# Optimization experiments

Hardware: AMD Instinct MI355X
Metric: run time of the kernel (lower is better)

The kernel has to match this reference:

```python
import jax, jax.numpy as jnp
from jax import lax
import numpy as np

B, T, D, H, FC, OUT = 256, 512, 64, 512, 512, 8


def _uniform(key, shape, scale):
    return jax.random.uniform(key, shape, jnp.float32, -scale, scale)


def setup_inputs() -> dict:
    key = jax.random.key(0)
    ks = jax.random.split(key, 16)
    s = 1.0 / np.sqrt(H)
    inp = {
        "x": jax.random.normal(ks[0], (B, T, D), jnp.float32),
        # LSTM layer 0 (PyTorch gate order i,f,g,o stacked along 4H)
        "W_ih0": _uniform(ks[1], (4 * H, D), s),
        "W_hh0": _uniform(ks[2], (4 * H, H), s),
        "b_ih0": _uniform(ks[3], (4 * H,), s),
        "b_hh0": _uniform(ks[4], (4 * H,), s),
        # LSTM layer 1
        "W_ih1": _uniform(ks[5], (4 * H, H), s),
        "W_hh1": _uniform(ks[6], (4 * H, H), s),
        "b_ih1": _uniform(ks[7], (4 * H,), s),
        "b_hh1": _uniform(ks[8], (4 * H,), s),
        # MLP head: Linear(H,FC) -> ReLU -> Linear(FC,OUT)
        "W_fc1": _uniform(ks[9], (FC, H), s),
        "b_fc1": _uniform(ks[10], (FC,), s),
        "W_fc2": _uniform(ks[11], (OUT, FC), 1.0 / np.sqrt(FC)),
        "b_fc2": _uniform(ks[12], (OUT,), 1.0 / np.sqrt(FC)),
    }
    return inp


def _lstm_layer(x, W_ih, W_hh, b_ih, b_hh):
    # x: [B, T, Din] -> hidden sequence [B, T, H]
    Bn, Tn, _ = x.shape
    Hn = W_hh.shape[1]
    # precompute input-to-gate projections for all timesteps (one big GEMM)
    xg = jnp.einsum('btd,gd->btg', x, W_ih) + b_ih + b_hh  # [B, T, 4H]

    def step(carry, xg_t):
        h, c = carry
        g = xg_t + h @ W_hh.T  # [B, 4H]
        i, f, gg, o = jnp.split(g, 4, axis=-1)
        c = jax.nn.sigmoid(f) * c + jax.nn.sigmoid(i) * jnp.tanh(gg)
        h = jax.nn.sigmoid(o) * jnp.tanh(c)
        return (h, c), h

    h0 = jnp.zeros((Bn, Hn), x.dtype)
    (_, _), hs = lax.scan(step, (h0, h0), jnp.swapaxes(xg, 0, 1))  # hs: [T, B, H]
    return jnp.swapaxes(hs, 0, 1)


def reference(x, W_ih0, W_hh0, b_ih0, b_hh0, W_ih1, W_hh1, b_ih1, b_hh1,
              W_fc1, b_fc1, W_fc2, b_fc2):
    h = _lstm_layer(x, W_ih0, W_hh0, b_ih0, b_hh0)
    h = _lstm_layer(h, W_ih1, W_hh1, b_ih1, b_hh1)
    last = h[:, -1, :]  # [B, H]
    z = jax.nn.relu(last @ W_fc1.T + b_fc1)
    return z @ W_fc2.T + b_fc2  # [B, OUT]
```

## Files before the change

kernel.cpp:

```cpp
#include <hip/hip_runtime.h>
#include <math.h>

typedef unsigned short u16;
typedef __attribute__((ext_vector_type(8))) short short8;
typedef __attribute__((ext_vector_type(4))) float float4v;

#define HH   512
#define BB   256
#define TLEN 512
#define DD   64

__device__ __forceinline__ float sigm(float x) { return 1.0f / (1.0f + __expf(-x)); }

__device__ __forceinline__ u16 bf16rn(float v) {
    unsigned u = __float_as_uint(v);
    u += 0x7fffu + ((u >> 16) & 1u);
    return (u16)(u >> 16);
}
__device__ __forceinline__ float bf16tf(u16 h) { return __uint_as_float(((unsigned)h) << 16); }


__global__ __launch_bounds__(256) void split_kernel(const float* __restrict__ src,
                                                    u16* __restrict__ hi, u16* __restrict__ lo, int n)
{
    for (int i = blockIdx.x * 256 + threadIdx.x; i < n; i += gridDim.x * 256) {
        float v = src[i];
        u16 h = bf16rn(v);
        hi[i] = h;
        lo[i] = bf16rn(v - bf16tf(h));
    }
}

__global__ __launch_bounds__(256) void zero_kernel(unsigned* p, int n)
{
    int i = blockIdx.x * 256 + threadIdx.x;
    if (i < n) p[i] = 0u;
}


template<int NKT, int C1, bool ROLE1>
__device__ void lstm_body(
    const u16* __restrict__ X1h, const u16* __restrict__ X1l,
    const u16* __restrict__ B1h, const u16* __restrict__ B1l, const int ldb1,
    const u16* __restrict__ B2h, const u16* __restrict__ B2l,
    const float* __restrict__ pbi, const float* __restrict__ pbh,
    u16* __restrict__ h0hA, u16* __restrict__ h0lA,
    u16* __restrict__ h0hB, u16* __restrict__ h0lB,
    u16* __restrict__ h1hA, u16* __restrict__ h1lA,
    u16* __restrict__ h1hB, u16* __restrict__ h1lB,
    float* __restrict__ h1last,
    unsigned* bcnt, unsigned* bgen,
    const int m0, const int j0, u16* smem)
{
    const int tid  = threadIdx.x;
    const int lane = tid & 63;
    const int wv   = tid >> 6;
    const int g    = wv & 3;
    const int kh   = wv >> 2;
    float* sX = (float*)smem;

    short8 rBh[NKT], rBl[NKT];
    {
        const size_t brow = (size_t)(g * HH + j0 + (lane & 15));
        const int kq = (lane >> 4) * 8;
#pragma unroll
        for (int i = 0; i < NKT; ++i) {
            const int kt = kh * NKT + i;
            const u16 *ph, *pl;
            if (kt < C1) {
                ph = B1h + brow * (size_t)ldb1 + kt * 32 + kq;
                pl = B1l + brow * (size_t)ldb1 + kt * 32 + kq;
            } else {
                ph = B2h + brow * HH + (size_t)(kt - C1) * 32 + kq;
                pl = B2l + brow * HH + (size_t)(kt - C1) * 32 + kq;
            }
            rBh[i] = *(const short8*)ph;
            rBl[i] = *(const short8*)pl;
        }
    }

    int r_[2], ks_[2], hl_[2], half_[2], loff_[2];
#pragma unroll
    for (int q = 0; q < 2; ++q) {
        const int idx  = q * 512 + tid;
        const int tile = idx >> 8;
        half_[q] = tile >> 1;
        hl_[q]   = tile & 1;
        const int t8 = idx & 255;
        const int r  = t8 >> 2;
        const int k3 = t8 & 3;
        r_[q]  = r;
        ks_[q] = k3 * 8;
        loff_[q] = tile * 2048 + r * 32 + ((k3 ^ ((r >> 1) & 3)) * 8);
    }

    const int cR = lane & 15, q4 = lane >> 4;
    const int abase = kh * 4096 + cR * 32 + ((q4 ^ ((cR >> 1) & 3)) * 8);

    const int jj  = j0 + (tid & 15);
    const int mb2 = (tid >> 4) * 2;
    const float bI = pbi[jj] + pbh[jj];
    const float bF = pbi[HH + jj] + pbh[HH + jj];
    const float bG = pbi[2 * HH + jj] + pbh[2 * HH + jj];
    const float bO = pbi[3 * HH + jj] + pbh[3 * HH + jj];
    float cst0 = 0.f, cst1 = 0.f;

    for (int n = 0; n <= TLEN; ++n) {
        const int rb = n & 1;
        const bool active = ROLE1 ? (n > 0) : (n < TLEN);
        if (active) {
            const u16 *A1h_, *A1l_, *A2h_, *A2l_;
            u16 *wh, *wl;
            size_t ld1;
            if (ROLE1) {
                A1h_ = rb ? h0hB : h0hA; A1l_ = rb ? h0lB : h0lA;
                A2h_ = rb ? h1hB : h1hA; A2l_ = rb ? h1lB : h1lA;
                wh   = rb ? h1hA : h1hB; wl   = rb ? h1lA : h1lB;
                ld1 = HH;
            } else {
                A1h_ = X1h + (size_t)n * DD; A1l_ = X1l + (size_t)n * DD;
                A2h_ = rb ? h0hB : h0hA;     A2l_ = rb ? h0lB : h0lA;
                wh   = rb ? h0hA : h0hB;     wl   = rb ? h0lA : h0lB;
                ld1 = (size_t)TLEN * DD;
            }

            auto srcp = [&](int kt, int r, int ks, int lo) -> const u16* {
                if (kt < C1) return (lo ? A1l_ : A1h_) + (size_t)(m0 + r) * ld1 + kt * 32 + ks;
                return (lo ? A2l_ : A2h_) + (size_t)(m0 + r) * HH + (size_t)(kt - C1) * 32 + ks;
            };

            float4v acc[4];
#pragma unroll
            for (int mt = 0; mt < 4; ++mt) acc[mt] = (float4v){0.f, 0.f, 0.f, 0.f};

            short8 vS[2][2];
            vS[0][0] = *(const short8*)srcp(half_[0] * NKT + 0, r_[0], ks_[0], hl_[0]);
            vS[0][1] = *(const short8*)srcp(half_[1] * NKT + 0, r_[1], ks_[1], hl_[1]);
            if (NKT > 1) {
                vS[1][0] = *(const short8*)srcp(half_[0] * NKT + 1, r_[0], ks_[0], hl_[0]);
                vS[1][1] = *(const short8*)srcp(half_[1] * NKT + 1, r_[1], ks_[1], hl_[1]);
            }
            *(short8*)&smem[loff_[0]] = vS[0][0];
            *(short8*)&smem[loff_[1]] = vS[0][1];

#pragma unroll
            for (int i = 0; i < NKT; ++i) {
                __syncthreads();
                const int buf = i & 1;
                if (i + 1 < NKT) {
                    *(short8*)&smem[(buf ^ 1) * 8192 + loff_[0]] = vS[(i + 1) & 1][0];
                    *(short8*)&smem[(buf ^ 1) * 8192 + loff_[1]] = vS[(i + 1) & 1][1];
                }
                if (i + 2 < NKT) {
                    vS[i & 1][0] = *(const short8*)srcp(half_[0] * NKT + i + 2, r_[0], ks_[0], hl_[0]);
                    vS[i & 1][1] = *(const short8*)srcp(half_[1] * NKT + i + 2, r_[1], ks_[1], hl_[1]);
                }
                const int ab = buf * 8192 + abase;
                short8 aH[4], aL[4];
#pragma unroll
                for (int mt = 0; mt < 4; ++mt) {
                    aH[mt] = *(const short8*)&smem[ab + mt * 512];
                    aL[mt] = *(const short8*)&smem[ab + 2048 + mt * 512];
                }
#pragma unroll
                for (int mt = 0; mt < 4; ++mt) {
                    acc[mt] = __builtin_amdgcn_mfma_f32_16x16x32_bf16(aH[mt], rBh[i], acc[mt], 0, 0, 0);
                    acc[mt] = __builtin_amdgcn_mfma_f32_16x16x32_bf16(aH[mt], rBl[i], acc[mt], 0, 0, 0);
                    acc[mt] = __builtin_amdgcn_mfma_f32_16x16x32_bf16(aL[mt], rBh[i], acc[mt], 0, 0, 0);
                }
            }

            __syncthreads();
#pragma unroll
            for (int mt = 0; mt < 4; ++mt)
#pragma unroll
                for (int r = 0; r < 4; ++r)
                    sX[wv * 1152 + (mt * 16 + (lane >> 4) * 4 + r) * 18 + (lane & 15)] = acc[mt][r];
            __syncthreads();

#pragma unroll
            for (int p = 0; p < 2; ++p) {
                const int m = mb2 + p;
                const int xb = m * 18 + (tid & 15);
                const float gi = sX[0 * 1152 + xb] + sX[4 * 1152 + xb] + bI;
                const float gf = sX[1 * 1152 + xb] + sX[5 * 1152 + xb] + bF;
                const float gg = sX[2 * 1152 + xb] + sX[6 * 1152 + xb] + bG;
                const float go = sX[3 * 1152 + xb] + sX[7 * 1152 + xb] + bO;
                const float cp = p ? cst1 : cst0;
                const float cn = sigm(gf) * cp + sigm(gi) * tanhf(gg);
                const float h  = sigm(go) * tanhf(cn);
                if (p) cst1 = cn; else cst0 = cn;
                const size_t off = (size_t)(m0 + m) * HH + jj;
                const u16 hv = bf16rn(h);
                wh[off] = hv;
                wl[off] = bf16rn(h - bf16tf(hv));
                if (ROLE1 && n == TLEN) h1last[off] = h;
            }
        }

        __syncthreads();
        if (tid == 0) {
            const unsigned g0 = __hip_atomic_load(bgen, __ATOMIC_RELAXED, __HIP_MEMORY_SCOPE_AGENT);
            const unsigned a = __hip_atomic_fetch_add(bcnt, 1u, __ATOMIC_RELEASE, __HIP_MEMORY_SCOPE_AGENT);
            if (a == 63u) {
                __hip_atomic_store(bcnt, 0u, __ATOMIC_RELAXED, __HIP_MEMORY_SCOPE_AGENT);
                __hip_atomic_store(bgen, g0 + 1u, __ATOMIC_RELEASE, __HIP_MEMORY_SCOPE_AGENT);
            } else {
                int sp = 0;
                while (__hip_atomic_load(bgen, __ATOMIC_RELAXED, __HIP_MEMORY_SCOPE_AGENT) == g0) {
                    __builtin_amdgcn_s_sleep(2);
                    if ((++sp & 63) == 0)
                        (void)__hip_atomic_load(bgen, __ATOMIC_ACQUIRE, __HIP_MEMORY_SCOPE_AGENT);
                }
            }
            (void)__hip_atomic_load(bgen, __ATOMIC_ACQUIRE, __HIP_MEMORY_SCOPE_AGENT);
        }
        __syncthreads();
    }
}

__global__ __launch_bounds__(512, 2) void lstm_persistent(
    const u16* __restrict__ xhi, const u16* __restrict__ xlo,
    const u16* __restrict__ Wih0h, const u16* __restrict__ Wih0l,
    const u16* __restrict__ Whh0h, const u16* __restrict__ Whh0l,
    const u16* __restrict__ Wih1h, const u16* __restrict__ Wih1l,
    const u16* __restrict__ Whh1h, const u16* __restrict__ Whh1l,
    const float* __restrict__ bi0, const float* __restrict__ bh0,
    const float* __restrict__ bi1, const float* __restrict__ bh1,
    u16* h0hA, u16* h0lA, u16* h0hB, u16* h0lB,
    u16* h1hA, u16* h1lA, u16* h1hB, u16* h1lB,
    float* __restrict__ h1last, unsigned* bar)
{
    __shared__ u16 smem[18432];
    const bool role1 = (blockIdx.x >= 128);
    const int idx = blockIdx.x & 127;
    const int m0 = (idx & 3) * 64;
    const int j0 = (idx >> 2) * 16;
    const int gid = idx & 3;
    unsigned* bcnt = bar + gid * 64;
    unsigned* bgen = bar + gid * 64 + 32;

    if (role1)
        lstm_body<16, 16, true>(nullptr, nullptr,
            Wih1h, Wih1l, HH, Whh1h, Whh1l, bi1, bh1,
            h0hA, h0lA, h0hB, h0lB, h1hA, h1lA, h1hB, h1lB,
            h1last, bcnt, bgen, m0, j0, smem);
    else
        lstm_body<9, 2, false>(xhi, xlo,
            Wih0h, Wih0l, DD, Whh0h, Whh0l, bi0, bh0,
            h0hA, h0lA, h0hB, h0lB, h1hA, h1lA, h1hB, h1lB,
            nullptr, bcnt, bgen, m0, j0, smem);
}


template <int MODE>
__global__ __launch_bounds__(256) void gemm_step(
    const float* __restrict__ A1, int lda1, int K1, const float* __restrict__ W1,
    const float* __restrict__ A2, int K2, const float* __restrict__ W2,
    const float* __restrict__ b1, const float* __restrict__ b2,
    const float* __restrict__ c_in, float* __restrict__ c_out,
    float* __restrict__ h_out)
{
    __shared__ float sA[16][33];
    __shared__ float sW[128][33];

    const int tid = threadIdx.x;
    const int tj  = tid & 31;
    const int tg  = tid >> 5;
    const int m0  = blockIdx.x * 16;
    const int j0  = blockIdx.y * ((MODE == 0) ? 32 : 128);

    float acc[2][4] = {{0.f, 0.f, 0.f, 0.f}, {0.f, 0.f, 0.f, 0.f}};

    for (int seg = 0; seg < 2; ++seg) {
        const float* A  = seg ? A2 : A1;
        const float* W  = seg ? W2 : W1;
        const int    K  = seg ? K2 : K1;
        const int    ld = seg ? HH : lda1;
        if (K == 0) continue;
        for (int kb = 0; kb < K; kb += 32) {
            __syncthreads();
            {
                int idxq = tid;
#pragma unroll
                for (int r = 0; r < 2; ++r, idxq += 256) {
                    int row = idxq >> 5, col = idxq & 31;
                    sA[row][col] = A[(m0 + row) * ld + kb + col];
                }
            }
            {
#pragma unroll
                for (int i = 0; i < 16; ++i) {
                    int idxq = i * 256 + tid;
                    int row = idxq >> 5, col = idxq & 31;
                    int grw;
                    if (MODE == 0) grw = (row >> 5) * HH + j0 + (row & 31);
                    else           grw = j0 + row;
                    sW[row][col] = W[grw * K + kb + col];
                }
            }
            __syncthreads();
#pragma unroll
            for (int k = 0; k < 32; ++k) {
                float a0 = sA[tg][k];
                float a1 = sA[tg + 8][k];
                float w0 = sW[tj][k];
                float w1 = sW[32 + tj][k];
                float w2 = sW[64 + tj][k];
                float w3 = sW[96 + tj][k];
                acc[0][0] += a0 * w0; acc[0][1] += a0 * w1;
                acc[0][2] += a0 * w2; acc[0][3] += a0 * w3;
                acc[1][0] += a1 * w0; acc[1][1] += a1 * w1;
                acc[1][2] += a1 * w2; acc[1][3] += a1 * w3;
            }
        }
    }

    if (MODE == 0) {
        const int j = j0 + tj;
        const float bi = b1[j] + b2[j];
        const float bf = b1[HH + j] + b2[HH + j];
        const float bg = b1[2 * HH + j] + b2[2 * HH + j];
        const float bo = b1[3 * HH + j] + b2[3 * HH + j];
#pragma unroll
        for (int r = 0; r < 2; ++r) {
            int m = m0 + tg + r * 8;
            float gi = acc[r][0] + bi;
            float gf = acc[r][1] + bf;
            float gg = acc[r][2] + bg;
            float go = acc[r][3] + bo;
            float cp = c_in[m * HH + j];
            float c  = sigm(gf) * cp + sigm(gi) * tanhf(gg);
            float h  = sigm(go) * tanhf(c);
            c_out[m * HH + j] = c;
            h_out[m * HH + j] = h;
        }
    } else {
#pragma unroll
        for (int r = 0; r < 2; ++r) {
            int m = m0 + tg + r * 8;
#pragma unroll
            for (int q = 0; q < 4; ++q) {
                int nn = j0 + q * 32 + tj;
                float v = acc[r][q] + b1[nn];
                h_out[m * HH + nn] = fmaxf(v, 0.f);
            }
        }
    }
}

__global__ __launch_bounds__(64) void fc2_kernel(
    const float* __restrict__ z, const float* __restrict__ W,
    const float* __restrict__ b, float* __restrict__ out)
{
    int m = blockIdx.x;
    int lane = threadIdx.x;
    float zr[8];
#pragma unroll
    for (int u = 0; u < 8; ++u) zr[u] = z[m * 512 + u * 64 + lane];
#pragma unroll
    for (int o = 0; o < 8; ++o) {
        float s = 0.f;
#pragma unroll
        for (int u = 0; u < 8; ++u) s += zr[u] * W[o * 512 + u * 64 + lane];
#pragma unroll
        for (int off = 32; off > 0; off >>= 1) s += __shfl_down(s, off);
        if (lane == 0) out[m * 8 + o] = s + b[o];
    }
}

__global__ __launch_bounds__(256) void zero_f_kernel(float* p, int n)
{
    int i = blockIdx.x * 256 + threadIdx.x;
    if (i < n) p[i] = 0.f;
}


extern "C" void kernel_launch(void* const* d_in, const int* in_sizes, int n_in,
                              void* d_out, int out_size, void* d_ws, size_t ws_size,
                              hipStream_t stream)
{
    const float* x     = (const float*)d_in[0];
    const float* W_ih0 = (const float*)d_in[1];
    const float* W_hh0 = (const float*)d_in[2];
    const float* b_ih0 = (const float*)d_in[3];
    const float* b_hh0 = (const float*)d_in[4];
    const float* W_ih1 = (const float*)d_in[5];
    const float* W_hh1 = (const float*)d_in[6];
    const float* b_ih1 = (const float*)d_in[7];
    const float* b_hh1 = (const float*)d_in[8];
    const float* W_fc1 = (const float*)d_in[9];
    const float* b_fc1 = (const float*)d_in[10];
    const float* W_fc2 = (const float*)d_in[11];
    const float* b_fc2 = (const float*)d_in[12];
    float* out = (float*)d_out;

    const size_t S  = (size_t)BB * HH;
    const size_t SB = S * sizeof(u16);
    const size_t SF = S * sizeof(float);
    const size_t XN = (size_t)BB * TLEN * DD;

    const size_t NEED = 2097152 + 1024  +
                        4 * SB  +
                        2 * SF  + 2 * XN * 2  +
                        2 * 131072 * 2  + 3 * 2 * 1048576 * 2 ;

    if (ws_size >= NEED) {
        char* W = (char*)d_ws;
        size_t o = 0;
        u16 *h0hi[2], *h0lo[2], *h1hi[2], *h1lo[2];
        h0hi[0] = (u16*)(W + o); o += SB;
        h0lo[0] = (u16*)(W + o); o += SB;
        h1hi[1] = (u16*)(W + o); o += SB;
        h1lo[1] = (u16*)(W + o); o += SB;
        float* pad0 = (float*)(W + o); o += SF;
        float* pad1 = (float*)(W + o); o += SF;
        unsigned* bar = (unsigned*)(W + o); o += 1024;
        (void)pad0; (void)pad1;
        h0hi[1] = (u16*)(W + o); o += SB;
        h0lo[1] = (u16*)(W + o); o += SB;
        h1hi[0] = (u16*)(W + o); o += SB;
        h1lo[0] = (u16*)(W + o); o += SB;
        float* h1last = (float*)(W + o); o += SF;
        float* zfc    = (float*)(W + o); o += SF;
        u16* xhi = (u16*)(W + o); o += XN * 2;
        u16* xlo = (u16*)(W + o); o += XN * 2;
        u16* wih0h = (u16*)(W + o); o += 131072 * 2;
        u16* wih0l = (u16*)(W + o); o += 131072 * 2;
        u16* whh0h = (u16*)(W + o); o += 1048576 * 2;
        u16* whh0l = (u16*)(W + o); o += 1048576 * 2;
        u16* wih1h = (u16*)(W + o); o += 1048576 * 2;
        u16* wih1l = (u16*)(W + o); o += 1048576 * 2;
        u16* whh1h = (u16*)(W + o); o += 1048576 * 2;
        u16* whh1l = (u16*)(W + o); o += 1048576 * 2;

        zero_kernel<<<2049, 256, 0, stream>>>((unsigned*)d_ws, 524544);
        split_kernel<<<2048, 256, 0, stream>>>(x, xhi, xlo, (int)XN);
        split_kernel<<<512, 256, 0, stream>>>(W_ih0, wih0h, wih0l, 131072);
        split_kernel<<<2048, 256, 0, stream>>>(W_hh0, whh0h, whh0l, 1048576);
        split_kernel<<<2048, 256, 0, stream>>>(W_ih1, wih1h, wih1l, 1048576);
        split_kernel<<<2048, 256, 0, stream>>>(W_hh1, whh1h, whh1l, 1048576);

        lstm_persistent<<<256, 512, 0, stream>>>(
            xhi, xlo,
            wih0h, wih0l, whh0h, whh0l,
            wih1h, wih1l, whh1h, whh1l,
            b_ih0, b_hh0, b_ih1, b_hh1,
            h0hi[0], h0lo[0], h0hi[1], h0lo[1],
            h1hi[0], h1lo[0], h1hi[1], h1lo[1],
            h1last, bar);

        dim3 grid_fc1(BB / 16, 512 / 128);
        gemm_step<1><<<grid_fc1, 256, 0, stream>>>(
            h1last, HH, HH, W_fc1, nullptr, 0, nullptr,
            b_fc1, nullptr, nullptr, nullptr, zfc);
        fc2_kernel<<<BB, 64, 0, stream>>>(zfc, W_fc2, b_fc2, out);
        return;
    }

    float* wsf = (float*)d_ws;
    float* h0a = wsf + 0 * S;
    float* c0  = wsf + 1 * S;
    float* h1a = wsf + 2 * S;
    float* c1  = wsf + 3 * S;
    float* h0b = wsf + 4 * S;
    float* h1b = wsf + 5 * S;
    float* zb  = wsf + 6 * S;
    float* h0buf[2] = {h0a, h0b};
    float* h1buf[2] = {h1a, h1b};

    zero_f_kernel<<<(int)((4 * S + 255) / 256), 256, 0, stream>>>(wsf, (int)(4 * S));

    dim3 grid_lstm(BB / 16, HH / 32);
    for (int t = 0; t < TLEN; ++t) {
        const float* xt = x + (size_t)t * DD;
        gemm_step<0><<<grid_lstm, 256, 0, stream>>>(
            xt, TLEN * DD, DD, W_ih0,
            h0buf[t & 1], HH, W_hh0,
            b_ih0, b_hh0, c0, c0, h0buf[(t + 1) & 1]);
        gemm_step<0><<<grid_lstm, 256, 0, stream>>>(
            h0buf[(t + 1) & 1], HH, HH, W_ih1,
            h1buf[t & 1], HH, W_hh1,
            b_ih1, b_hh1, c1, c1, h1buf[(t + 1) & 1]);
    }
    dim3 grid_fc1(BB / 16, 512 / 128);
    gemm_step<1><<<grid_fc1, 256, 0, stream>>>(
        h1buf[0], HH, HH, W_fc1, nullptr, 0, nullptr,
        b_fc1, nullptr, nullptr, nullptr, zb);
    fc2_kernel<<<BB, 64, 0, stream>>>(zb, W_fc2, b_fc2, out);
}
```

Measured before the change: 7.322 ms.

## Split LSTM K across four wave quads with async LDS loads and hierarchical barrier

```diff
diff --git a/kernel.cpp b/kernel.cpp
--- a/kernel.cpp
+++ b/kernel.cpp
@@ -38,7 +38,7 @@
 }
 
 
-template<int NKT, int C1, bool ROLE1>
+template<int NCH, int C1, bool ROLE1>
 __device__ void lstm_body(
     const u16* __restrict__ X1h, const u16* __restrict__ X1l,
     const u16* __restrict__ B1h, const u16* __restrict__ B1l, const int ldb1,
@@ -49,61 +49,63 @@
     u16* __restrict__ h1hA, u16* __restrict__ h1lA,
     u16* __restrict__ h1hB, u16* __restrict__ h1lB,
     float* __restrict__ h1last,
-    unsigned* bcnt, unsigned* bgen,
+    unsigned* bar_g, const int aid,
     const int m0, const int j0, u16* smem)
 {
     const int tid  = threadIdx.x;
     const int lane = tid & 63;
     const int wv   = tid >> 6;
-    const int g    = wv & 3;
-    const int kh   = wv >> 2;
-    float* sX = (float*)smem;
-
-    short8 rBh[NKT], rBl[NKT];
+    const int q    = wv & 3;
+    const int gp   = wv >> 2;
+
+    constexpr int QB = NCH / 4, QR = NCH % 4;
+    constexpr int NKTMAX = (NCH + 3) / 4;
+    const int cntq = QB + (q < QR ? 1 : 0);
+    const int stq  = q * QB + (q < QR ? q : QR);
+
+    char* smemB = (char*)smem;
+
+    short8 rBh[2][NKTMAX], rBl[2][NKTMAX];
     {
-        const size_t brow = (size_t)(g * HH + j0 + (lane & 15));
-        const int kq = (lane >> 4) * 8;
-#pragma unroll
-        for (int i = 0; i < NKT; ++i) {
-            const int kt = kh * NKT + i;
-            const u16 *ph, *pl;
-            if (kt < C1) {
-                ph = B1h + brow * (size_t)ldb1 + kt * 32 + kq;
-                pl = B1l + brow * (size_t)ldb1 + kt * 32 + kq;
-            } else {
-                ph = B2h + brow * HH + (size_t)(kt - C1) * 32 + kq;
-                pl = B2l + brow * HH + (size_t)(kt - C1) * 32 + kq;
-            }
-            rBh[i] = *(const short8*)ph;
-            rBl[i] = *(const short8*)pl;
+        const int kq8 = (lane >> 4) * 8;
+#pragma unroll
+        for (int gg = 0; gg < 2; ++gg) {
+            const size_t brow = (size_t)((gp * 2 + gg) * HH + j0 + (lane & 15));
+#pragma unroll
+            for (int i = 0; i < NKTMAX; ++i) {
+                if (i < cntq) {
+                    const int kt = stq + i;
+                    const u16 *ph, *pl;
+                    if (kt < C1) {
+                        ph = B1h + brow * (size_t)ldb1 + kt * 32 + kq8;
+                        pl = B1l + brow * (size_t)ldb1 + kt * 32 + kq8;
+                    } else {
+                        ph = B2h + brow * HH + (size_t)(kt - C1) * 32 + kq8;
+                        pl = B2l + brow * HH + (size_t)(kt - C1) * 32 + kq8;
+                    }
+                    rBh[gg][i] = *(const short8*)ph;
+                    rBl[gg][i] = *(const short8*)pl;
+                }
+            }
         }
     }
 
-    int r_[2], ks_[2], hl_[2], half_[2], loff_[2];
-#pragma unroll
-    for (int q = 0; q < 2; ++q) {
-        const int idx  = q * 512 + tid;
-        const int tile = idx >> 8;
-        half_[q] = tile >> 1;
-        hl_[q]   = tile & 1;
-        const int t8 = idx & 255;
-        const int r  = t8 >> 2;
-        const int k3 = t8 & 3;
-        r_[q]  = r;
-        ks_[q] = k3 * 8;
-        loff_[q] = tile * 2048 + r * 32 + ((k3 ^ ((r >> 1) & 3)) * 8);
-    }
-
-    const int cR = lane & 15, q4 = lane >> 4;
-    const int abase = kh * 4096 + cR * 32 + ((q4 ^ ((cR >> 1) & 3)) * 8);
+    const int r0     = lane >> 2;
+    const int ksubst = (((lane & 3) ^ ((lane >> 3) & 3)) * 8);
+    const int abyte  = (lane & 15) * 64 + (((lane >> 4) ^ (((lane & 15) >> 1) & 3)) * 16);
 
     const int jj  = j0 + (tid & 15);
+    const int jl  = tid & 15;
     const int mb2 = (tid >> 4) * 2;
     const float bI = pbi[jj] + pbh[jj];
     const float bF = pbi[HH + jj] + pbh[HH + jj];
     const float bG = pbi[2 * HH + jj] + pbh[2 * HH + jj];
     const float bO = pbi[3 * HH + jj] + pbh[3 * HH + jj];
     float cst0 = 0.f, cst1 = 0.f;
+
+    unsigned* subp = bar_g + (aid >> 3) * 16;
+    unsigned* topp = bar_g + 128;
+    unsigned* genp = bar_g + 144;
 
     for (int n = 0; n <= TLEN; ++n) {
         const int rb = n & 1;
@@ -124,70 +126,113 @@
                 ld1 = (size_t)TLEN * DD;
             }
 
-            auto srcp = [&](int kt, int r, int ks, int lo) -> const u16* {
-                if (kt < C1) return (lo ? A1l_ : A1h_) + (size_t)(m0 + r) * ld1 + kt * 32 + ks;
-                return (lo ? A2l_ : A2h_) + (size_t)(m0 + r) * HH + (size_t)(kt - C1) * 32 + ks;
+            auto stage = [&](int kt, int bufoff) {
+                const u16* base; size_t ld; int ko;
+                if (kt < C1) { base = gp ? A1l_ : A1h_; ld = ld1; ko = kt * 32; }
+                else         { base = gp ? A2l_ : A2h_; ld = HH;  ko = (kt - C1) * 32; }
+                const u16* src = base + (size_t)(m0 + r0) * ld + ko + ksubst;
+                char* ldsb = smemB + bufoff + q * 8192 + gp * 4096;
+#pragma unroll
+                for (int j = 0; j < 4; ++j) {
+                    __builtin_amdgcn_global_load_lds(
+                        (const __attribute__((address_space(1))) unsigned int*)(src + (size_t)j * 16 * ld),
+                        (__attribute__((address_space(3))) unsigned int*)(ldsb + j * 1024),
+                        16, 0, 0);
+                }
             };
 
-            float4v acc[4];
-#pragma unroll
-            for (int mt = 0; mt < 4; ++mt) acc[mt] = (float4v){0.f, 0.f, 0.f, 0.f};
-
-            short8 vS[2][2];
-            vS[0][0] = *(const short8*)srcp(half_[0] * NKT + 0, r_[0], ks_[0], hl_[0]);
-            vS[0][1] = *(const short8*)srcp(half_[1] * NKT + 0, r_[1], ks_[1], hl_[1]);
-            if (NKT > 1) {
-                vS[1][0] = *(const short8*)srcp(half_[0] * NKT + 1, r_[0], ks_[0], hl_[0]);
-                vS[1][1] = *(const short8*)srcp(half_[1] * NKT + 1, r_[1], ks_[1], hl_[1]);
-            }
-            *(short8*)&smem[loff_[0]] = vS[0][0];
-            *(short8*)&smem[loff_[1]] = vS[0][1];
-
-#pragma unroll
-            for (int i = 0; i < NKT; ++i) {
+            float4v acc[2][4];
+#pragma unroll
+            for (int gg = 0; gg < 2; ++gg)
+#pragma unroll
+                for (int mt = 0; mt < 4; ++mt) acc[gg][mt] = (float4v){0.f, 0.f, 0.f, 0.f};
+
+            stage(stq, 0);
+            __syncthreads();
+
+#pragma unroll
+            for (int i = 0; i < NKTMAX; ++i) {
+                if (i + 1 < cntq) stage(stq + i + 1, ((i + 1) & 1) * 32768);
+                if (i < cntq) {
+                    const int bb = (i & 1) * 32768 + q * 8192;
+                    short8 aH[4], aL[4];
+#pragma unroll
+                    for (int mt = 0; mt < 4; ++mt) {
+                        aH[mt] = *(const short8*)(smemB + bb + mt * 1024 + abyte);
+                        aL[mt] = *(const short8*)(smemB + bb + 4096 + mt * 1024 + abyte);
+                    }
+#pragma unroll
+                    for (int gg = 0; gg < 2; ++gg)
+#pragma unroll
+                        for (int mt = 0; mt < 4; ++mt) {
+                            acc[gg][mt] = __builtin_amdgcn_mfma_f32_16x16x32_bf16(aH[mt], rBh[gg][i], acc[gg][mt], 0, 0, 0);
+                            acc[gg][mt] = __builtin_amdgcn_mfma_f32_16x16x32_bf16(aH[mt], rBl[gg][i], acc[gg][mt], 0, 0, 0);
+                            acc[gg][mt] = __builtin_amdgcn_mfma_f32_16x16x32_bf16(aL[mt], rBh[gg][i], acc[gg][mt], 0, 0, 0);
+                        }
+                }
                 __syncthreads();
-                const int buf = i & 1;
-                if (i + 1 < NKT) {
-                    *(short8*)&smem[(buf ^ 1) * 8192 + loff_[0]] = vS[(i + 1) & 1][0];
-                    *(short8*)&smem[(buf ^ 1) * 8192 + loff_[1]] = vS[(i + 1) & 1][1];
-                }
-                if (i + 2 < NKT) {
-                    vS[i & 1][0] = *(const short8*)srcp(half_[0] * NKT + i + 2, r_[0], ks_[0], hl_[0]);
-                    vS[i & 1][1] = *(const short8*)srcp(half_[1] * NKT + i + 2, r_[1], ks_[1], hl_[1]);
-                }
-                const int ab = buf * 8192 + abase;
-                short8 aH[4], aL[4];
-#pragma unroll
-                for (int mt = 0; mt < 4; ++mt) {
-                    aH[mt] = *(const short8*)&smem[ab + mt * 512];
-                    aL[mt] = *(const short8*)&smem[ab + 2048 + mt * 512];
-                }
-#pragma unroll
-                for (int mt = 0; mt < 4; ++mt) {
-                    acc[mt] = __builtin_amdgcn_mfma_f32_16x16x32_bf16(aH[mt], rBh[i], acc[mt], 0, 0, 0);
-                    acc[mt] = __builtin_amdgcn_mfma_f32_16x16x32_bf16(aH[mt], rBl[i], acc[mt], 0, 0, 0);
-                    acc[mt] = __builtin_amdgcn_mfma_f32_16x16x32_bf16(aL[mt], rBh[i], acc[mt], 0, 0, 0);
-                }
-            }
-
+            }
+
+            if (q & 1) {
+                char* p = smemB + (((gp << 1) | (q >> 1)) * 8192) + lane * 16;
+#pragma unroll
+                for (int gg = 0; gg < 2; ++gg)
+#pragma unroll
+                    for (int mt = 0; mt < 4; ++mt)
+                        *(float4v*)(p + (gg * 4 + mt) * 1024) = acc[gg][mt];
+            }
             __syncthreads();
-#pragma unroll
-            for (int mt = 0; mt < 4; ++mt)
-#pragma unroll
-                for (int r = 0; r < 4; ++r)
-                    sX[wv * 1152 + (mt * 16 + (lane >> 4) * 4 + r) * 18 + (lane & 15)] = acc[mt][r];
+            if (!(q & 1)) {
+                char* p = smemB + (((gp << 1) | (q >> 1)) * 8192) + lane * 16;
+#pragma unroll
+                for (int gg = 0; gg < 2; ++gg)
+#pragma unroll
+                    for (int mt = 0; mt < 4; ++mt)
+                        acc[gg][mt] += *(const float4v*)(p + (gg * 4 + mt) * 1024);
+                if (q == 2) {
+                    char* p2 = smemB + 32768 + gp * 8192 + lane * 16;
+#pragma unroll
+                    for (int gg = 0; gg < 2; ++gg)
+#pragma unroll
+                        for (int mt = 0; mt < 4; ++mt)
+                            *(float4v*)(p2 + (gg * 4 + mt) * 1024) = acc[gg][mt];
+                }
+            }
+            __syncthreads();
+            if (q == 0) {
+                char* p2 = smemB + 32768 + gp * 8192 + lane * 16;
+#pragma unroll
+                for (int gg = 0; gg < 2; ++gg)
+#pragma unroll
+                    for (int mt = 0; mt < 4; ++mt)
+                        acc[gg][mt] += *(const float4v*)(p2 + (gg * 4 + mt) * 1024);
+                const int jw = lane & 15, qw = lane >> 4;
+#pragma unroll
+                for (int gg = 0; gg < 2; ++gg)
+#pragma unroll
+                    for (int mt = 0; mt < 4; ++mt) {
+                        const int g = gp * 2 + gg;
+                        const int s = mt * 4 + qw;
+                        *(float4v*)(smemB + 49152 +
+                            (((g * 16 + jw) * 16) + (s ^ (jw & 7))) * 16) = acc[gg][mt];
+                    }
+            }
             __syncthreads();
 
 #pragma unroll
             for (int p = 0; p < 2; ++p) {
                 const int m = mb2 + p;
-                const int xb = m * 18 + (tid & 15);
-                const float gi = sX[0 * 1152 + xb] + sX[4 * 1152 + xb] + bI;
-                const float gf = sX[1 * 1152 + xb] + sX[5 * 1152 + xb] + bF;
-                const float gg = sX[2 * 1152 + xb] + sX[6 * 1152 + xb] + bG;
-                const float go = sX[3 * 1152 + xb] + sX[7 * 1152 + xb] + bO;
+                float gv[4];
+#pragma unroll
+                for (int g = 0; g < 4; ++g)
+                    gv[g] = *(const float*)(smemB + 49152 +
+                        (((g * 16 + jl) * 16) + ((m >> 2) ^ (jl & 7))) * 16 + (m & 3) * 4);
+                const float gi = gv[0] + bI;
+                const float gf = gv[1] + bF;
+                const float gG = gv[2] + bG;
+                const float go = gv[3] + bO;
                 const float cp = p ? cst1 : cst0;
-                const float cn = sigm(gf) * cp + sigm(gi) * tanhf(gg);
+                const float cn = sigm(gf) * cp + sigm(gi) * tanhf(gG);
                 const float h  = sigm(go) * tanhf(cn);
                 if (p) cst1 = cn; else cst0 = cn;
                 const size_t off = (size_t)(m0 + m) * HH + jj;
@@ -200,20 +245,23 @@
 
         __syncthreads();
         if (tid == 0) {
-            const unsigned g0 = __hip_atomic_load(bgen, __ATOMIC_RELAXED, __HIP_MEMORY_SCOPE_AGENT);
-            const unsigned a = __hip_atomic_fetch_add(bcnt, 1u, __ATOMIC_RELEASE, __HIP_MEMORY_SCOPE_AGENT);
-            if (a == 63u) {
-                __hip_atomic_store(bcnt, 0u, __ATOMIC_RELAXED, __HIP_MEMORY_SCOPE_AGENT);
-                __hip_atomic_store(bgen, g0 + 1u, __ATOMIC_RELEASE, __HIP_MEMORY_SCOPE_AGENT);
-            } else {
-                int sp = 0;
-                while (__hip_atomic_load(bgen, __ATOMIC_RELAXED, __HIP_MEMORY_SCOPE_AGENT) == g0) {
-                    __builtin_amdgcn_s_sleep(2);
-                    if ((++sp & 63) == 0)
-                        (void)__hip_atomic_load(bgen, __ATOMIC_ACQUIRE, __HIP_MEMORY_SCOPE_AGENT);
-                }
-            }
-            (void)__hip_atomic_load(bgen, __ATOMIC_ACQUIRE, __HIP_MEMORY_SCOPE_AGENT);
+            const unsigned g0 = __hip_atomic_load(genp, __ATOMIC_RELAXED, __HIP_MEMORY_SCOPE_AGENT);
+            const unsigned a = __hip_atomic_fetch_add(subp, 1u, __ATOMIC_ACQ_REL, __HIP_MEMORY_SCOPE_AGENT);
+            if (a == 7u) {
+                __hip_atomic_store(subp, 0u, __ATOMIC_RELAXED, __HIP_MEMORY_SCOPE_AGENT);
+                const unsigned t = __hip_atomic_fetch_add(topp, 1u, __ATOMIC_ACQ_REL, __HIP_MEMORY_SCOPE_AGENT);
+                if (t == 7u) {
+                    __hip_atomic_store(topp, 0u, __ATOMIC_RELAXED, __HIP_MEMORY_SCOPE_AGENT);
+                    __hip_atomic_store(genp, g0 + 1u, __ATOMIC_RELEASE, __HIP_MEMORY_SCOPE_AGENT);
+                }
+            }
+            int sp = 0;
+            while (__hip_atomic_load(genp, __ATOMIC_RELAXED, __HIP_MEMORY_SCOPE_AGENT) == g0) {
+                __builtin_amdgcn_s_sleep(1);
+                if ((++sp & 63) == 0)
+                    (void)__hip_atomic_load(genp, __ATOMIC_ACQUIRE, __HIP_MEMORY_SCOPE_AGENT);
+            }
+            (void)__hip_atomic_load(genp, __ATOMIC_ACQUIRE, __HIP_MEMORY_SCOPE_AGENT);
         }
         __syncthreads();
     }
@@ -231,25 +279,25 @@
     u16* h1hA, u16* h1lA, u16* h1hB, u16* h1lB,
     float* __restrict__ h1last, unsigned* bar)
 {
-    __shared__ u16 smem[18432];
+    __shared__ u16 smem[32768];
     const bool role1 = (blockIdx.x >= 128);
     const int idx = blockIdx.x & 127;
     const int m0 = (idx & 3) * 64;
     const int j0 = (idx >> 2) * 16;
     const int gid = idx & 3;
-    unsigned* bcnt = bar + gid * 64;
-    unsigned* bgen = bar + gid * 64 + 32;
+    unsigned* bar_g = bar + gid * 256;
+    const int aid = (role1 ? 32 : 0) + (idx >> 2);
 
     if (role1)
-        lstm_body<16, 16, true>(nullptr, nullptr,
+        lstm_body<32, 16, true>(nullptr, nullptr,
             Wih1h, Wih1l, HH, Whh1h, Whh1l, bi1, bh1,
             h0hA, h0lA, h0hB, h0lB, h1hA, h1lA, h1hB, h1lB,
-            h1last, bcnt, bgen, m0, j0, smem);
+            h1last, bar_g, aid, m0, j0, smem);
     else
-        lstm_body<9, 2, false>(xhi, xlo,
+        lstm_body<18, 2, false>(xhi, xlo,
             Wih0h, Wih0l, DD, Whh0h, Whh0l, bi0, bh0,
             h0hA, h0lA, h0hB, h0lB, h1hA, h1lA, h1hB, h1lB,
-            nullptr, bcnt, bgen, m0, j0, smem);
+            nullptr, bar_g, aid, m0, j0, smem);
 }
 
 
@@ -400,7 +448,8 @@
     const size_t SF = S * sizeof(float);
     const size_t XN = (size_t)BB * TLEN * DD;
 
-    const size_t NEED = 2097152 + 1024  +
+    const size_t ZERO = 4 * SB + 2 * SF + 4096;
+    const size_t NEED = ZERO +
                         4 * SB  +
                         2 * SF  + 2 * XN * 2  +
                         2 * 131072 * 2  + 3 * 2 * 1048576 * 2 ;
@@ -415,7 +464,7 @@
         h1lo[1] = (u16*)(W + o); o += SB;
         float* pad0 = (float*)(W + o); o += SF;
         float* pad1 = (float*)(W + o); o += SF;
-        unsigned* bar = (unsigned*)(W + o); o += 1024;
+        unsigned* bar = (unsigned*)(W + o); o += 4096;
         (void)pad0; (void)pad1;
         h0hi[1] = (u16*)(W + o); o += SB;
         h0lo[1] = (u16*)(W + o); o += SB;
@@ -434,7 +483,7 @@
         u16* whh1h = (u16*)(W + o); o += 1048576 * 2;
         u16* whh1l = (u16*)(W + o); o += 1048576 * 2;
 
-        zero_kernel<<<2049, 256, 0, stream>>>((unsigned*)d_ws, 524544);
+        zero_kernel<<<2052, 256, 0, stream>>>((unsigned*)d_ws, (int)(ZERO / 4));
         split_kernel<<<2048, 256, 0, stream>>>(x, xhi, xlo, (int)XN);
         split_kernel<<<512, 256, 0, stream>>>(W_ih0, wih0h, wih0l, 131072);
         split_kernel<<<2048, 256, 0, stream>>>(W_hh0, whh0h, whh0l, 1048576);
```

Result: slower. 16.88 ms (+130.6%).

## Replace group barrier with per-role monotonic counters and triple-buffered layer-0 hidden state

Applied to the files above, without the earlier changes.

```diff
diff --git a/kernel.cpp b/kernel.cpp
--- a/kernel.cpp
+++ b/kernel.cpp
@@ -18,6 +18,9 @@
     return (u16)(u >> 16);
 }
 __device__ __forceinline__ float bf16tf(u16 h) { return __uint_as_float(((unsigned)h) << 16); }
+
+template <typename T>
+__device__ __forceinline__ T sel3(int i, T a, T b, T c) { return i == 0 ? a : (i == 1 ? b : c); }
 
 
 __global__ __launch_bounds__(256) void split_kernel(const float* __restrict__ src,
@@ -44,12 +47,13 @@
     const u16* __restrict__ B1h, const u16* __restrict__ B1l, const int ldb1,
     const u16* __restrict__ B2h, const u16* __restrict__ B2l,
     const float* __restrict__ pbi, const float* __restrict__ pbh,
-    u16* __restrict__ h0hA, u16* __restrict__ h0lA,
-    u16* __restrict__ h0hB, u16* __restrict__ h0lB,
+    u16* __restrict__ h0h0, u16* __restrict__ h0l0,
+    u16* __restrict__ h0h1, u16* __restrict__ h0l1,
+    u16* __restrict__ h0h2, u16* __restrict__ h0l2,
     u16* __restrict__ h1hA, u16* __restrict__ h1lA,
     u16* __restrict__ h1hB, u16* __restrict__ h1lB,
     float* __restrict__ h1last,
-    unsigned* bcnt, unsigned* bgen,
+    unsigned* bc0, unsigned* bc1,
     const int m0, const int j0, u16* smem)
 {
     const int tid  = threadIdx.x;
@@ -106,21 +110,46 @@
     float cst0 = 0.f, cst1 = 0.f;
 
     for (int n = 0; n <= TLEN; ++n) {
-        const int rb = n & 1;
+        if (tid == 0) {
+            const unsigned tOwn = 32u * (unsigned)n;
+            const unsigned tOth = ROLE1 ? 32u * (unsigned)n
+                                        : (n >= 1 ? 32u * (unsigned)(n - 1) : 0u);
+            unsigned* own = ROLE1 ? bc1 : bc0;
+            unsigned* oth = ROLE1 ? bc0 : bc1;
+            int sp = 0;
+            for (;;) {
+                unsigned vo = __hip_atomic_load(own, __ATOMIC_RELAXED, __HIP_MEMORY_SCOPE_AGENT);
+                unsigned vt = __hip_atomic_load(oth, __ATOMIC_RELAXED, __HIP_MEMORY_SCOPE_AGENT);
+                if (vo >= tOwn && vt >= tOth) break;
+                __builtin_amdgcn_s_sleep(2);
+                if ((++sp & 63) == 0)
+                    (void)__hip_atomic_load(own, __ATOMIC_ACQUIRE, __HIP_MEMORY_SCOPE_AGENT);
+            }
+            (void)__hip_atomic_load(own, __ATOMIC_ACQUIRE, __HIP_MEMORY_SCOPE_AGENT);
+        }
+        __syncthreads();
+
         const bool active = ROLE1 ? (n > 0) : (n < TLEN);
         if (active) {
+            const int rb   = n & 1;
+            const int rbuf = (n + 2) % 3;
+            const int wbuf = n % 3;
+
             const u16 *A1h_, *A1l_, *A2h_, *A2l_;
             u16 *wh, *wl;
             size_t ld1;
             if (ROLE1) {
-                A1h_ = rb ? h0hB : h0hA; A1l_ = rb ? h0lB : h0lA;
+                A1h_ = sel3<const u16*>(rbuf, h0h0, h0h1, h0h2);
+                A1l_ = sel3<const u16*>(rbuf, h0l0, h0l1, h0l2);
                 A2h_ = rb ? h1hB : h1hA; A2l_ = rb ? h1lB : h1lA;
                 wh   = rb ? h1hA : h1hB; wl   = rb ? h1lA : h1lB;
                 ld1 = HH;
             } else {
                 A1h_ = X1h + (size_t)n * DD; A1l_ = X1l + (size_t)n * DD;
-                A2h_ = rb ? h0hB : h0hA;     A2l_ = rb ? h0lB : h0lA;
-                wh   = rb ? h0hA : h0hB;     wl   = rb ? h0lA : h0lB;
+                A2h_ = sel3<const u16*>(rbuf, h0h0, h0h1, h0h2);
+                A2l_ = sel3<const u16*>(rbuf, h0l0, h0l1, h0l2);
+                wh   = sel3<u16*>(wbuf, h0h0, h0h1, h0h2);
+                wl   = sel3<u16*>(wbuf, h0l0, h0l1, h0l2);
                 ld1 = (size_t)TLEN * DD;
             }
 
@@ -199,22 +228,8 @@
         }
 
         __syncthreads();
-        if (tid == 0) {
-            const unsigned g0 = __hip_atomic_load(bgen, __ATOMIC_RELAXED, __HIP_MEMORY_SCOPE_AGENT);
-            const unsigned a = __hip_atomic_fetch_add(bcnt, 1u, __ATOMIC_RELEASE, __HIP_MEMORY_SCOPE_AGENT);
-            if (a == 63u) {
-                __hip_atomic_store(bcnt, 0u, __ATOMIC_RELAXED, __HIP_MEMORY_SCOPE_AGENT);
-                __hip_atomic_store(bgen, g0 + 1u, __ATOMIC_RELEASE, __HIP_MEMORY_SCOPE_AGENT);
-            } else {
-                int sp = 0;
-                while (__hip_atomic_load(bgen, __ATOMIC_RELAXED, __HIP_MEMORY_SCOPE_AGENT) == g0) {
-                    __builtin_amdgcn_s_sleep(2);
-                    if ((++sp & 63) == 0)
-                        (void)__hip_atomic_load(bgen, __ATOMIC_ACQUIRE, __HIP_MEMORY_SCOPE_AGENT);
-                }
-            }
-            (void)__hip_atomic_load(bgen, __ATOMIC_ACQUIRE, __HIP_MEMORY_SCOPE_AGENT);
-        }
+        if (tid == 0)
+            __hip_atomic_fetch_add(ROLE1 ? bc1 : bc0, 1u, __ATOMIC_RELEASE, __HIP_MEMORY_SCOPE_AGENT);
         __syncthreads();
     }
 }
@@ -227,8 +242,8 @@
     const u16* __restrict__ Whh1h, const u16* __restrict__ Whh1l,
     const float* __restrict__ bi0, const float* __restrict__ bh0,
     const float* __restrict__ bi1, const float* __restrict__ bh1,
-    u16* h0hA, u16* h0lA, u16* h0hB, u16* h0lB,
-    u16* h1hA, u16* h1lA, u16* h1hB, u16* h1lB,
+    u16* h0h0_, u16* h0l0_, u16* h0h1_, u16* h0l1_, u16* h0h2_, u16* h0l2_,
+    u16* h1h0_, u16* h1l0_, u16* h1h1_, u16* h1l1_,
     float* __restrict__ h1last, unsigned* bar)
 {
     __shared__ u16 smem[18432];
@@ -237,19 +252,21 @@
     const int m0 = (idx & 3) * 64;
     const int j0 = (idx >> 2) * 16;
     const int gid = idx & 3;
-    unsigned* bcnt = bar + gid * 64;
-    unsigned* bgen = bar + gid * 64 + 32;
+    unsigned* bc0 = bar + gid * 64;
+    unsigned* bc1 = bar + gid * 64 + 32;
 
     if (role1)
         lstm_body<16, 16, true>(nullptr, nullptr,
             Wih1h, Wih1l, HH, Whh1h, Whh1l, bi1, bh1,
-            h0hA, h0lA, h0hB, h0lB, h1hA, h1lA, h1hB, h1lB,
-            h1last, bcnt, bgen, m0, j0, smem);
+            h0h0_, h0l0_, h0h1_, h0l1_, h0h2_, h0l2_,
+            h1h0_, h1l0_, h1h1_, h1l1_,
+            h1last, bc0, bc1, m0, j0, smem);
     else
         lstm_body<9, 2, false>(xhi, xlo,
             Wih0h, Wih0l, DD, Whh0h, Whh0l, bi0, bh0,
-            h0hA, h0lA, h0hB, h0lB, h1hA, h1lA, h1hB, h1lB,
-            nullptr, bcnt, bgen, m0, j0, smem);
+            h0h0_, h0l0_, h0h1_, h0l1_, h0h2_, h0l2_,
+            h1h0_, h1l0_, h1h1_, h1l1_,
+            nullptr, bc0, bc1, m0, j0, smem);
 }
 
 
@@ -400,23 +417,22 @@
     const size_t SF = S * sizeof(float);
     const size_t XN = (size_t)BB * TLEN * DD;
 
-    const size_t NEED = 2097152 + 1024  +
-                        4 * SB  +
+    const size_t ZERO = 4 * SB + 1024;
+    const size_t NEED = ZERO + 6 * SB  +
                         2 * SF  + 2 * XN * 2  +
                         2 * 131072 * 2  + 3 * 2 * 1048576 * 2 ;
 
     if (ws_size >= NEED) {
         char* W = (char*)d_ws;
         size_t o = 0;
-        u16 *h0hi[2], *h0lo[2], *h1hi[2], *h1lo[2];
+        u16 *h0hi[3], *h0lo[3], *h1hi[2], *h1lo[2];
+        h0hi[2] = (u16*)(W + o); o += SB;
+        h0lo[2] = (u16*)(W + o); o += SB;
+        h1hi[1] = (u16*)(W + o); o += SB;
+        h1lo[1] = (u16*)(W + o); o += SB;
+        unsigned* bar = (unsigned*)(W + o); o += 1024;
         h0hi[0] = (u16*)(W + o); o += SB;
         h0lo[0] = (u16*)(W + o); o += SB;
-        h1hi[1] = (u16*)(W + o); o += SB;
-        h1lo[1] = (u16*)(W + o); o += SB;
-        float* pad0 = (float*)(W + o); o += SF;
-        float* pad1 = (float*)(W + o); o += SF;
-        unsigned* bar = (unsigned*)(W + o); o += 1024;
-        (void)pad0; (void)pad1;
         h0hi[1] = (u16*)(W + o); o += SB;
         h0lo[1] = (u16*)(W + o); o += SB;
         h1hi[0] = (u16*)(W + o); o += SB;
@@ -434,7 +450,7 @@
         u16* whh1h = (u16*)(W + o); o += 1048576 * 2;
         u16* whh1l = (u16*)(W + o); o += 1048576 * 2;
 
-        zero_kernel<<<2049, 256, 0, stream>>>((unsigned*)d_ws, 524544);
+        zero_kernel<<<1025, 256, 0, stream>>>((unsigned*)d_ws, (int)(ZERO / 4));
         split_kernel<<<2048, 256, 0, stream>>>(x, xhi, xlo, (int)XN);
         split_kernel<<<512, 256, 0, stream>>>(W_ih0, wih0h, wih0l, 131072);
         split_kernel<<<2048, 256, 0, stream>>>(W_hh0, whh0h, whh0l, 1048576);
@@ -446,7 +462,7 @@
             wih0h, wih0l, whh0h, whh0l,
             wih1h, wih1l, whh1h, whh1l,
             b_ih0, b_hh0, b_ih1, b_hh1,
-            h0hi[0], h0lo[0], h0hi[1], h0lo[1],
+            h0hi[0], h0lo[0], h0hi[1], h0lo[1], h0hi[2], h0lo[2],
             h1hi[0], h1lo[0], h1hi[1], h1lo[1],
             h1last, bar);
 
```

Measured after the change: 8.389 ms. +14.6%, slower.
